# Performance work log

Measured on AMD Instinct MI355X. Metric: run time of the kernel, lower is better.

The kernel has to match this reference:

```python
import jax, jax.numpy as jnp
import numpy as np

B = 4096
D = 128
TEMP = 0.5
EPS = 1e-8  # torch cosine_similarity norm clamp


def setup_inputs() -> dict:
    key = jax.random.key(0)
    k1, k2 = jax.random.split(key)
    zi = jax.random.normal(k1, (B, D), dtype=jnp.float32)
    zj = jax.random.normal(k2, (B, D), dtype=jnp.float32)
    return {"zi": zi, "zj": zj}


def reference(zi, zj):
    b = zi.shape[0]
    n2 = 2 * b
    z = jnp.concatenate([zi, zj], axis=0)                      # (2N, D)
    norm = jnp.maximum(jnp.linalg.norm(z, axis=-1, keepdims=True), EPS)
    zn = z / norm
    sim = zn @ zn.T                                            # (2N, 2N) cosine similarity
    # positives: torch.diag(sim, +B) and torch.diag(sim, -B)
    right = jnp.diagonal(sim, offset=b)                        # sim[i, i+B]
    left = jnp.diagonal(sim, offset=-b)                        # sim[i+B, i]
    pos = jnp.concatenate([left, right]) / TEMP                # (2N,)
    # logits row i = [pos_i] + all sims except self-diagonal and the positive,
    # so the softmax denominator set = all entries except the self-diagonal.
    logits = sim / TEMP
    neg_big = jnp.asarray(jnp.finfo(logits.dtype).min, logits.dtype)
    masked = jnp.where(jnp.eye(n2, dtype=bool), neg_big, logits)
    lse = jax.nn.logsumexp(masked, axis=1)                     # (2N,)
    # CrossEntropyLoss(reduction='sum') with label 0, then / 2N
    loss = jnp.sum(lse - pos) / n2
    return loss
```

## Files before the change

### kernel.cpp

```cpp
#include <hip/hip_runtime.h>
#include <hip/hip_bf16.h>


#define BB 4096
#define N2 8192
#define DD 128
#define CSPLIT 32
#define CW (N2 / CSPLIT)
#define TW 64
#define NRD (CW / TW)

#define SCALE 1.69864360f

#if __has_builtin(__builtin_amdgcn_exp2f)
#define EXP2F(x) __builtin_amdgcn_exp2f(x)
#else
#define EXP2F(x) __expf((x) * 0.6931471805599453f)
#endif

using bf16 = __hip_bfloat16;
typedef __attribute__((ext_vector_type(8))) short short8;
typedef __attribute__((ext_vector_type(4))) float float4v;

__global__ __launch_bounds__(256) void ntx_norm_kernel(
    const float* __restrict__ zi, const float* __restrict__ zj,
    bf16* __restrict__ zn, float* __restrict__ rowsum, float* __restrict__ pos) {
  const int wave = threadIdx.x >> 6;
  const int lane = threadIdx.x & 63;
  const int pair = blockIdx.x * 4 + wave;
  float2 v = ((const float2*)(zi + (size_t)pair * DD))[lane];
  float2 w = ((const float2*)(zj + (size_t)pair * DD))[lane];
  float s1 = v.x * v.x + v.y * v.y;
  float s2 = w.x * w.x + w.y * w.y;
  float s3 = v.x * w.x + v.y * w.y;
  #pragma unroll
  for (int o = 32; o > 0; o >>= 1) {
    s1 += __shfl_xor(s1, o);
    s2 += __shfl_xor(s2, o);
    s3 += __shfl_xor(s3, o);
  }
  float nv = fmaxf(sqrtf(s1), 1e-8f);
  float nw = fmaxf(sqrtf(s2), 1e-8f);
  float rv = SCALE / nv, rw = SCALE / nw;
  bf16 bx = __float2bfloat16(v.x * rv);
  bf16 by = __float2bfloat16(v.y * rv);
  bf16 cx = __float2bfloat16(w.x * rw);
  bf16 cy = __float2bfloat16(w.y * rw);
  __hip_bfloat162 h2; h2.x = bx; h2.y = by;
  __hip_bfloat162 g2; g2.x = cx; g2.y = cy;
  ((__hip_bfloat162*)(zn + (size_t)pair * DD))[lane] = h2;
  ((__hip_bfloat162*)(zn + (size_t)(pair + BB) * DD))[lane] = g2;
  float fx = __bfloat162float(bx), fy = __bfloat162float(by);
  float gx = __bfloat162float(cx), gy = __bfloat162float(cy);
  float sii = fx * fx + fy * fy;
  float sjj = gx * gx + gy * gy;
  #pragma unroll
  for (int o = 32; o > 0; o >>= 1) {
    sii += __shfl_xor(sii, o);
    sjj += __shfl_xor(sjj, o);
  }
  if (lane == 0) {
    float c = s3 / (nv * nw);
    rowsum[pair]      = -EXP2F(sii);
    rowsum[pair + BB] = -EXP2F(sjj);
    pos[pair]      = c;
    pos[pair + BB] = c;
  }
}

__global__ __launch_bounds__(256) void ntx_sim_kernel(
    const bf16* __restrict__ zn, float* __restrict__ rowsum) {
  const int tid  = threadIdx.x;
  const int wave = tid >> 6;
  const int lane = tid & 63;
  const int quad = lane >> 4;
  const int l15  = lane & 15;
  const char* zb  = (const char*)zn;
  const short* zs = (const short*)zn;

  __shared__ float4 lds[2][TW * 16];

  const int rowBase  = blockIdx.y * 256 + wave * 64;
  const int colBase0 = blockIdx.x * CW;

  const int g0 = tid >> 4;
  const int sw = ((tid & 15) ^ (g0 & 7)) << 4;
  const char* srcb = zb + (size_t)(colBase0 + g0) * 256 + sw;

  float4 p0 = *(const float4*)(srcb);
  float4 p1 = *(const float4*)(srcb + 4096);
  float4 p2 = *(const float4*)(srcb + 8192);
  float4 p3 = *(const float4*)(srcb + 12288);

  short8 a[4][4];
  #pragma unroll
  for (int t = 0; t < 4; t++) {
    const short* ap = zs + (size_t)(rowBase + t * 16 + l15) * DD + quad * 8;
    #pragma unroll
    for (int c = 0; c < 4; c++) a[t][c] = *(const short8*)(ap + c * 32);
  }
  asm volatile("" : "+v"(a[0][0]), "+v"(a[0][1]), "+v"(a[0][2]), "+v"(a[0][3]),
                    "+v"(a[1][0]), "+v"(a[1][1]), "+v"(a[1][2]), "+v"(a[1][3]),
                    "+v"(a[2][0]), "+v"(a[2][1]), "+v"(a[2][2]), "+v"(a[2][3]),
                    "+v"(a[3][0]), "+v"(a[3][1]), "+v"(a[3][2]), "+v"(a[3][3]));

  float rs[4][4];
  #pragma unroll
  for (int t = 0; t < 4; t++)
    #pragma unroll
    for (int r = 0; r < 4; r++) rs[t][r] = 0.0f;

  lds[0][tid] = p0;
  lds[0][tid + 256] = p1;
  lds[0][tid + 512] = p2;
  lds[0][tid + 768] = p3;
  __syncthreads();

  int cur = 0;
  #pragma unroll 1
  for (int rd = 0; rd < NRD; rd++) {
    float4 t0, t1, t2, t3;
    const bool pf = (rd + 1 < NRD);
    if (pf) {
      const char* sb = srcb + (size_t)(rd + 1) * (TW * 256);
      t0 = *(const float4*)(sb);
      t1 = *(const float4*)(sb + 4096);
      t2 = *(const float4*)(sb + 8192);
      t3 = *(const float4*)(sb + 12288);
    }

    const char* lb = (const char*)&lds[cur][0];
    #pragma unroll
    for (int k = 0; k < 4; k++) {
      short8 b[4];
      #pragma unroll
      for (int c = 0; c < 4; c++) {
        const int off = k * 4096 + l15 * 256 +
                        ((((c * 4 + quad) ^ (l15 & 7))) << 4);
        b[c] = *(const short8*)(lb + off);
      }
      #pragma unroll
      for (int t = 0; t < 4; t++) {
        float4v acc = {0.f, 0.f, 0.f, 0.f};
        acc = __builtin_amdgcn_mfma_f32_16x16x32_bf16(a[t][0], b[0], acc, 0, 0, 0);
        acc = __builtin_amdgcn_mfma_f32_16x16x32_bf16(a[t][1], b[1], acc, 0, 0, 0);
        acc = __builtin_amdgcn_mfma_f32_16x16x32_bf16(a[t][2], b[2], acc, 0, 0, 0);
        acc = __builtin_amdgcn_mfma_f32_16x16x32_bf16(a[t][3], b[3], acc, 0, 0, 0);
        #pragma unroll
        for (int r = 0; r < 4; r++) rs[t][r] += EXP2F(acc[r]);
      }
    }

    if (pf) {
      lds[cur ^ 1][tid] = t0;
      lds[cur ^ 1][tid + 256] = t1;
      lds[cur ^ 1][tid + 512] = t2;
      lds[cur ^ 1][tid + 768] = t3;
      __syncthreads();
      cur ^= 1;
    }
  }

  #pragma unroll
  for (int t = 0; t < 4; t++) {
    #pragma unroll
    for (int r = 0; r < 4; r++) {
      float s = rs[t][r];
      s += __shfl_xor(s, 1);
      s += __shfl_xor(s, 2);
      s += __shfl_xor(s, 4);
      s += __shfl_xor(s, 8);
      if (l15 == 0)
        atomicAdd(&rowsum[rowBase + t * 16 + quad * 4 + r], s);
    }
  }
}

__global__ __launch_bounds__(1024) void ntx_finalize_kernel(
    const float* __restrict__ rowsum, const float* __restrict__ pos,
    float* __restrict__ out) {
  float s = 0.f;
  for (int i = threadIdx.x; i < N2; i += 1024)
    s += __logf(rowsum[i]) - 2.0f * pos[i];
  #pragma unroll
  for (int o = 32; o > 0; o >>= 1) s += __shfl_xor(s, o);
  __shared__ float sm[16];
  const int wave = threadIdx.x >> 6;
  const int lane = threadIdx.x & 63;
  if (lane == 0) sm[wave] = s;
  __syncthreads();
  if (threadIdx.x == 0) {
    float t = 0.f;
    #pragma unroll
    for (int i = 0; i < 16; i++) t += sm[i];
    out[0] = t / (float)N2;
  }
}

extern "C" void kernel_launch(void* const* d_in, const int* in_sizes, int n_in,
                              void* d_out, int out_size, void* d_ws, size_t ws_size,
                              hipStream_t stream) {
  const float* zi = (const float*)d_in[0];
  const float* zj = (const float*)d_in[1];
  float* out = (float*)d_out;

  char* ws = (char*)d_ws;
  bf16* zn = (bf16*)ws;
  float* rowsum = (float*)(ws + (size_t)N2 * DD * 2);
  float* pos = rowsum + N2;

  ntx_norm_kernel<<<BB / 4, 256, 0, stream>>>(zi, zj, zn, rowsum, pos);
  dim3 grid(CSPLIT, N2 / 256);
  ntx_sim_kernel<<<grid, 256, 0, stream>>>(zn, rowsum);
  ntx_finalize_kernel<<<1, 1024, 0, stream>>>(rowsum, pos, out);
}
```

Before: 90.12 us.

## Stream B tiles per-wave via direct global-to-LDS loads, drop block barriers

Each wave now loads its own 16-column B tile straight from global memory into a private double-buffered LDS region using global_load_lds, replacing the register-staged shared tile and the block-wide __syncthreads. Waiting on vmcnt per iteration replaces block synchronization. This removes the register round trip and the cross-wave barriers, at the cost of each wave fetching B redundantly (4x the global/L2 traffic) and much finer-grained iterations.

```diff
diff --git a/kernel.cpp b/kernel.cpp
--- a/kernel.cpp
+++ b/kernel.cpp
@@ -7,8 +7,7 @@
 #define DD 128
 #define CSPLIT 32
 #define CW (N2 / CSPLIT)
-#define TW 64
-#define NRD (CW / TW)
+#define NCT (CW / 16)
 
 #define SCALE 1.69864360f
 
@@ -21,6 +20,12 @@
 using bf16 = __hip_bfloat16;
 typedef __attribute__((ext_vector_type(8))) short short8;
 typedef __attribute__((ext_vector_type(4))) float float4v;
+
+__device__ __forceinline__ void gl_lds16(const char* g, char* ldst) {
+  __builtin_amdgcn_global_load_lds(
+      (const __attribute__((address_space(1))) void*)g,
+      (__attribute__((address_space(3))) void*)ldst, 16, 0, 0);
+}
 
 __global__ __launch_bounds__(256) void ntx_norm_kernel(
     const float* __restrict__ zi, const float* __restrict__ zj,
@@ -78,19 +83,22 @@
   const char* zb  = (const char*)zn;
   const short* zs = (const short*)zn;
 
-  __shared__ float4 lds[2][TW * 16];
-
-  const int rowBase  = blockIdx.y * 256 + wave * 64;
-  const int colBase0 = blockIdx.x * CW;
-
-  const int g0 = tid >> 4;
-  const int sw = ((tid & 15) ^ (g0 & 7)) << 4;
-  const char* srcb = zb + (size_t)(colBase0 + g0) * 256 + sw;
-
-  float4 p0 = *(const float4*)(srcb);
-  float4 p1 = *(const float4*)(srcb + 4096);
-  float4 p2 = *(const float4*)(srcb + 8192);
-  float4 p3 = *(const float4*)(srcb + 12288);
+  __shared__ float4 lds[2048];
+
+  const int rowBase = blockIdx.y * 256 + wave * 64;
+  const int colBase = blockIdx.x * CW;
+
+  const int gr = lane >> 4;
+  const int sl = lane & 15;
+  const char* spE = zb + (size_t)(colBase + gr) * 256 + ((sl ^ gr) << 4);
+  const char* spO = zb + (size_t)(colBase + gr) * 256 + ((sl ^ (4 + gr)) << 4);
+
+  char* wb = (char*)lds + wave * 8192;
+
+  gl_lds16(spE,        wb);
+  gl_lds16(spO + 1024, wb + 1024);
+  gl_lds16(spE + 2048, wb + 2048);
+  gl_lds16(spO + 3072, wb + 3072);
 
   short8 a[4][4];
   #pragma unroll
@@ -110,55 +118,42 @@
     #pragma unroll
     for (int r = 0; r < 4; r++) rs[t][r] = 0.0f;
 
-  lds[0][tid] = p0;
-  lds[0][tid + 256] = p1;
-  lds[0][tid + 512] = p2;
-  lds[0][tid + 768] = p3;
-  __syncthreads();
-
-  int cur = 0;
+  asm volatile("s_waitcnt vmcnt(0)" ::: "memory");
+  __builtin_amdgcn_sched_barrier(0);
+
   #pragma unroll 1
-  for (int rd = 0; rd < NRD; rd++) {
-    float4 t0, t1, t2, t3;
-    const bool pf = (rd + 1 < NRD);
-    if (pf) {
-      const char* sb = srcb + (size_t)(rd + 1) * (TW * 256);
-      t0 = *(const float4*)(sb);
-      t1 = *(const float4*)(sb + 4096);
-      t2 = *(const float4*)(sb + 8192);
-      t3 = *(const float4*)(sb + 12288);
-    }
-
-    const char* lb = (const char*)&lds[cur][0];
-    #pragma unroll
-    for (int k = 0; k < 4; k++) {
-      short8 b[4];
+  for (int rd = 0; rd < NCT; rd++) {
+    const int cur = rd & 1;
+    char* cb = wb + cur * 4096;
+
+    if (rd + 1 < NCT) {
+      const size_t ro = (size_t)(rd + 1) * 4096;
+      char* nb = wb + (cur ^ 1) * 4096;
+      gl_lds16(spE + ro,        nb);
+      gl_lds16(spO + ro + 1024, nb + 1024);
+      gl_lds16(spE + ro + 2048, nb + 2048);
+      gl_lds16(spO + ro + 3072, nb + 3072);
+    }
+
+    short8 b[4];
+    #pragma unroll
+    for (int c = 0; c < 4; c++) {
+      const int off = l15 * 256 + ((((c * 4 + quad)) ^ (l15 & 7)) << 4);
+      b[c] = *(const short8*)(cb + off);
+    }
+    #pragma unroll
+    for (int t = 0; t < 4; t++) {
+      float4v acc = {0.f, 0.f, 0.f, 0.f};
+      acc = __builtin_amdgcn_mfma_f32_16x16x32_bf16(a[t][0], b[0], acc, 0, 0, 0);
+      acc = __builtin_amdgcn_mfma_f32_16x16x32_bf16(a[t][1], b[1], acc, 0, 0, 0);
+      acc = __builtin_amdgcn_mfma_f32_16x16x32_bf16(a[t][2], b[2], acc, 0, 0, 0);
+      acc = __builtin_amdgcn_mfma_f32_16x16x32_bf16(a[t][3], b[3], acc, 0, 0, 0);
       #pragma unroll
-      for (int c = 0; c < 4; c++) {
-        const int off = k * 4096 + l15 * 256 +
-                        ((((c * 4 + quad) ^ (l15 & 7))) << 4);
-        b[c] = *(const short8*)(lb + off);
-      }
-      #pragma unroll
-      for (int t = 0; t < 4; t++) {
-        float4v acc = {0.f, 0.f, 0.f, 0.f};
-        acc = __builtin_amdgcn_mfma_f32_16x16x32_bf16(a[t][0], b[0], acc, 0, 0, 0);
-        acc = __builtin_amdgcn_mfma_f32_16x16x32_bf16(a[t][1], b[1], acc, 0, 0, 0);
-        acc = __builtin_amdgcn_mfma_f32_16x16x32_bf16(a[t][2], b[2], acc, 0, 0, 0);
-        acc = __builtin_amdgcn_mfma_f32_16x16x32_bf16(a[t][3], b[3], acc, 0, 0, 0);
-        #pragma unroll
-        for (int r = 0; r < 4; r++) rs[t][r] += EXP2F(acc[r]);
-      }
-    }
-
-    if (pf) {
-      lds[cur ^ 1][tid] = t0;
-      lds[cur ^ 1][tid + 256] = t1;
-      lds[cur ^ 1][tid + 512] = t2;
-      lds[cur ^ 1][tid + 768] = t3;
-      __syncthreads();
-      cur ^= 1;
-    }
+      for (int r = 0; r < 4; r++) rs[t][r] += EXP2F(acc[r]);
+    }
+
+    asm volatile("s_waitcnt vmcnt(0)" ::: "memory");
+    __builtin_amdgcn_sched_barrier(0);
   }
 
   #pragma unroll
```

Result: slower. 93.20 us (+3.4%).
